# Performance work log

Hardware: AMD Instinct MI355X
Metric: run time of the kernel (lower is better)

Reference implementation:

```python
import jax, jax.numpy as jnp
import numpy as np

B, S, D, H = 4, 2048, 1024, 16
DH = D // H


def setup_inputs() -> dict:
    key = jax.random.key(0)
    ks = jax.random.split(key, 6)
    scale = 1.0 / np.sqrt(D)  # xavier-ish scale for weights
    return {
        "x": jax.random.normal(ks[0], (B, S, D), dtype=jnp.float32),
        "M": jax.random.normal(ks[1], (B, D, D), dtype=jnp.float32) * scale,
        "mask": jnp.zeros((1, 1, S, S), dtype=jnp.float32),
        "Wq": jax.random.normal(ks[2], (D, D), dtype=jnp.float32) * scale,
        "Wk": jax.random.normal(ks[3], (D, D), dtype=jnp.float32) * scale,
        "Wv": jax.random.normal(ks[4], (D, D), dtype=jnp.float32) * scale,
        "Wo": jax.random.normal(ks[5], (D, D), dtype=jnp.float32) * scale,
    }


def reference(x, M, mask, Wq, Wk, Wv, Wo):
    # Projections (torch Linear: y = x @ W^T, bias=False)
    Q = jnp.einsum('bsd,ed->bse', x, Wq)
    K = jnp.einsum('bsd,ed->bse', x, Wk)
    V = jnp.einsum('bsd,ed->bse', x, Wv)
    # Archetypal metric: QM = Q @ M, per-batch bilinear transform on full d_model
    QM = jnp.einsum('bsd,bde->bse', Q, M)

    def split(t):  # [B,S,D] -> [B,H,S,DH]
        return t.reshape(B, S, H, DH).transpose(0, 2, 1, 3)

    QMh, Kh, Vh = split(QM), split(K), split(V)
    scores = jnp.einsum('bhsd,bhtd->bhst', QMh, Kh) / np.sqrt(DH)
    scores = jnp.clip(scores, -50.0, 50.0)
    scores = scores + mask  # broadcast additive mask
    attn = jax.nn.softmax(scores, axis=-1)  # dropout is identity (eval)
    out = jnp.einsum('bhst,bhtd->bhsd', attn, Vh)
    out = out.transpose(0, 2, 1, 3).reshape(B, S, D)  # merge heads
    return jnp.einsum('bsd,ed->bse', out, Wo)
```

## Files before the change

kernel.cpp:

```cpp
#include <hip/hip_runtime.h>
#include <cstdint>

typedef __attribute__((ext_vector_type(8))) short short8;
typedef __attribute__((ext_vector_type(8))) __bf16 bf16x8;
typedef __attribute__((ext_vector_type(4))) float f32x4;

__device__ __forceinline__ uint32_t cvt_pk_bf16(float lo, float hi) {
  uint32_t r;
  asm("v_cvt_pk_bf16_f32 %0, %1, %2" : "=v"(r) : "v"(lo), "v"(hi));
  return r;
}

__device__ __forceinline__ short f2bf(float f) {
  return (short)cvt_pk_bf16(f, f);
}

__device__ __forceinline__ float exp2_fast(float x) {
  return __builtin_amdgcn_exp2f(x);
}

__device__ __forceinline__ void mem_fence_compiler() {
  asm volatile("" ::: "memory");
}

__device__ __forceinline__ void gload_lds16(const void* g, void* l) {
  __builtin_amdgcn_global_load_lds(
      (const __attribute__((address_space(1))) void*)(uintptr_t)g,
      (__attribute__((address_space(3))) void*)(uint32_t)(uintptr_t)l,
      16, 0, 0);
}


__global__ __launch_bounds__(256) void cvt_f32_bf16(const float* __restrict__ s,
                                                    short* __restrict__ d, long n) {
  long i = ((long)blockIdx.x * 256 + threadIdx.x) * 8;
  if (i + 8 > n) return;
  const float4 a = *(const float4*)(s + i);
  const float4 b = *(const float4*)(s + i + 4);
  uint4 o;
  o.x = cvt_pk_bf16(a.x, a.y);
  o.y = cvt_pk_bf16(a.z, a.w);
  o.z = cvt_pk_bf16(b.x, b.y);
  o.w = cvt_pk_bf16(b.z, b.w);
  *(uint4*)(d + i) = o;
}

__global__ __launch_bounds__(256) void cvt3_f32_bf16(
    const float* __restrict__ s0, short* __restrict__ d0,
    const float* __restrict__ s1, short* __restrict__ d1,
    const float* __restrict__ s2, short* __restrict__ d2) {
  const int which = blockIdx.x >> 9;
  const long i = (((long)(blockIdx.x & 511)) * 256 + threadIdx.x) * 8;
  const float* s = which == 0 ? s0 : (which == 1 ? s1 : s2);
  short* d = which == 0 ? d0 : (which == 1 ? d1 : d2);
  const float4 a = *(const float4*)(s + i);
  const float4 b = *(const float4*)(s + i + 4);
  uint4 o;
  o.x = cvt_pk_bf16(a.x, a.y);
  o.y = cvt_pk_bf16(a.z, a.w);
  o.z = cvt_pk_bf16(b.x, b.y);
  o.w = cvt_pk_bf16(b.z, b.w);
  *(uint4*)(d + i) = o;
}

__global__ __launch_bounds__(256) void cvtT5(const float* __restrict__ Wq,
                                             short* __restrict__ wqt,
                                             const float* __restrict__ M,
                                             short* __restrict__ Mt) {
  __shared__ short t[64][65];
  const int tid = threadIdx.x;
  const int z = blockIdx.z;
  const float* src = z == 0 ? Wq : M + (long)(z - 1) * 1024 * 1024;
  short* dst = z == 0 ? wqt : Mt + (long)(z - 1) * 1024 * 1024;
  const int d0 = blockIdx.x * 64, e0 = blockIdx.y * 64;
#pragma unroll
  for (int k = 0; k < 16; ++k) {
    int idx = k * 256 + tid; int r = idx >> 6, c = idx & 63;
    t[r][c] = f2bf(src[(long)(d0 + r) * 1024 + e0 + c]);
  }
  __syncthreads();
#pragma unroll
  for (int k = 0; k < 16; ++k) {
    int idx = k * 256 + tid; int r = idx >> 6, c = idx & 63;
    dst[(long)(e0 + r) * 1024 + d0 + c] = t[c][r];
  }
}

__global__ __launch_bounds__(256) void mask_flags(const float* __restrict__ mask,
                                                  int* __restrict__ flags) {
  __shared__ int f;
  const int tid = threadIdx.x;
  if (tid == 0) f = 0;
  __syncthreads();
  const int qt = blockIdx.x, tt = blockIdx.y;
  const float* base = mask + (long)qt * 64 * 2048 + tt * 64;
  const int r = tid >> 2, c = (tid & 3) * 16;
  bool nz = false;
#pragma unroll
  for (int k = 0; k < 4; ++k) {
    float4 v = *(const float4*)(base + (long)r * 2048 + c + k * 4);
    nz = nz | (v.x != 0.f) | (v.y != 0.f) | (v.z != 0.f) | (v.w != 0.f);
  }
  if (nz) f = 1;
  __syncthreads();
  if (tid == 0) flags[qt * 32 + tt] = f;
}


template <typename CT>
__global__ __launch_bounds__(256) void gemm_bt(
    const short* __restrict__ A, const short* __restrict__ B, CT* __restrict__ C,
    int M, int N, int K, long sA, long sB, long sC, float scale,
    short* __restrict__ vt) {
  __shared__ __align__(16) short pool[24576];
  short* Asb = pool;
  short* Bsb = pool + 12288;
  const int tid = threadIdx.x;
  const int w = tid >> 6, lane = tid & 63;
  const int wr = w >> 1, wc = w & 1;
  const int g = lane >> 4;
  const short* Ab = A + (long)blockIdx.z * sA + (long)blockIdx.x * 128 * K;
  const short* Bb = B + (long)blockIdx.z * sB + (long)blockIdx.y * 128 * K;

  f32x4 acc[4][4];
#pragma unroll
  for (int i = 0; i < 4; ++i)
#pragma unroll
    for (int j = 0; j < 4; ++j) acc[i][j] = {0.f, 0.f, 0.f, 0.f};

  const int srow = lane >> 2;
  const int scol = ((lane & 3) ^ (srow & 3)) * 8;

  auto STAGE = [&](int bufi, int k0) {
#pragma unroll
    for (int c = 0; c < 2; ++c) {
      const int chunk = w * 2 + c;
      const long gr = (long)(chunk * 16 + srow);
      gload_lds16(Ab + gr * K + k0 + scol, Asb + bufi * 4096 + chunk * 512);
      gload_lds16(Bb + gr * K + k0 + scol, Bsb + bufi * 4096 + chunk * 512);
    }
  };

  auto COMPUTE = [&](int bufi) {
    bf16x8 af[4], bfr[4];
#pragma unroll
    for (int mf = 0; mf < 4; ++mf) {
      const int r = wr * 64 + mf * 16 + (lane & 15);
      const int cb = g ^ (r & 3);
      af[mf] = *(const bf16x8*)&Asb[bufi * 4096 + r * 32 + cb * 8];
    }
#pragma unroll
    for (int nf = 0; nf < 4; ++nf) {
      const int r = wc * 64 + nf * 16 + (lane & 15);
      const int cb = g ^ (r & 3);
      bfr[nf] = *(const bf16x8*)&Bsb[bufi * 4096 + r * 32 + cb * 8];
    }
#pragma unroll
    for (int mf = 0; mf < 4; ++mf)
#pragma unroll
      for (int nf = 0; nf < 4; ++nf)
        acc[mf][nf] =
            __builtin_amdgcn_mfma_f32_16x16x32_bf16(af[mf], bfr[nf], acc[mf][nf], 0, 0, 0);
  };

  const int NK = K >> 5;
  STAGE(0, 0);
  if (NK > 1) STAGE(1, 32);
  for (int it = 0; it < NK; ++it) {
    const int cur = it % 3;
    if (it + 2 < NK) {
      STAGE((it + 2) % 3, (it + 2) * 32);
      asm volatile("s_waitcnt vmcnt(8)" ::: "memory");
    } else if (it + 1 < NK) {
      asm volatile("s_waitcnt vmcnt(4)" ::: "memory");
    } else {
      asm volatile("s_waitcnt vmcnt(0)" ::: "memory");
    }
    __builtin_amdgcn_s_barrier();
    __builtin_amdgcn_sched_barrier(0);
    COMPUTE(cur);
    __builtin_amdgcn_sched_barrier(0);
    __builtin_amdgcn_s_barrier();
  }

  const int r0 = g * 4, cc = lane & 15;
  if (vt != nullptr && blockIdx.z == 1) {
    __syncthreads();
#pragma unroll
    for (int mf = 0; mf < 4; ++mf)
#pragma unroll
      for (int i = 0; i < 4; ++i) {
        const int srow_l = wr * 64 + mf * 16 + r0 + i;
#pragma unroll
        for (int nf = 0; nf < 4; ++nf) {
          const int dh_l = wc * 64 + nf * 16 + cc;
          pool[dh_l * 136 + srow_l] = f2bf(acc[mf][nf][i]);
        }
      }
    __syncthreads();
    const long bb = blockIdx.x >> 4;
    const int s0b = (blockIdx.x & 15) * 128;
    const int hbase = blockIdx.y * 2;
#pragma unroll
    for (int pass = 0; pass < 4; ++pass) {
      const int dhrow = pass * 32 + (tid >> 3);
      const long vrow = (bb * 16 + hbase + (dhrow >> 6)) * 64 + (dhrow & 63);
      const int cseg = (tid & 7) * 16;
      bf16x8 v0 = *(const bf16x8*)&pool[dhrow * 136 + cseg];
      bf16x8 v1 = *(const bf16x8*)&pool[dhrow * 136 + cseg + 8];
      *(bf16x8*)(vt + vrow * 2048 + s0b + cseg) = v0;
      *(bf16x8*)(vt + vrow * 2048 + s0b + cseg + 8) = v1;
    }
    return;
  }

  CT* Cb = C + (long)blockIdx.z * sC;
#pragma unroll
  for (int mf = 0; mf < 4; ++mf)
#pragma unroll
    for (int i = 0; i < 4; ++i) {
      const long row = (long)blockIdx.x * 128 + wr * 64 + mf * 16 + r0 + i;
#pragma unroll
      for (int nf = 0; nf < 4; ++nf) {
        const long col = (long)blockIdx.y * 128 + wc * 64 + nf * 16 + cc;
        float v = acc[mf][nf][i] * scale;
        if constexpr (__is_same(CT, short))
          Cb[row * (long)N + col] = f2bf(v);
        else
          Cb[row * (long)N + col] = v;
      }
    }
}


__global__ __launch_bounds__(512) void flash_attn(
    const short* __restrict__ QM, const short* __restrict__ Kb,
    const short* __restrict__ Vt, const float* __restrict__ mask,
    const int* __restrict__ mflags, short* __restrict__ AO) {
  constexpr int S = 2048, D = 1024, NT = S / 64;
  constexpr float LOG2E = 1.44269504088896f;
  constexpr float CLIP = 50.0f * LOG2E;
  __shared__ __align__(16) short Ks[2][64 * 64];
  __shared__ __align__(16) short Vs[2][64 * 64];
  __shared__ __align__(16) short Ps[8][16 * 64];
  const int tid = threadIdx.x;
  const int w = tid >> 6, lane = tid & 63;
  const int q = lane & 15, g = lane >> 4;
  const int q0 = blockIdx.x * 128;
  const int h = blockIdx.y;
  const long b = blockIdx.z;

  const short* QMb = QM + (b * S) * D + h * 64;
  const short* Kbp = Kb + (b * S) * D + h * 64;
  const short* Vtp = Vt + ((b * 16 + h) * 64) * S;
  const int* flagrow = mflags + ((q0 + w * 16) >> 6) * 32;

  bf16x8 qf[2];
#pragma unroll
  for (int ks = 0; ks < 2; ++ks)
    qf[ks] = *(const bf16x8*)(QMb + (long)(q0 + w * 16 + q) * D + ks * 32 + g * 8);

  bf16x8 onesf;
#pragma unroll
  for (int j = 0; j < 8; ++j) onesf[j] = (__bf16)1.0f;

  f32x4 acc[4];
#pragma unroll
  for (int f = 0; f < 4; ++f) acc[f] = {0.f, 0.f, 0.f, 0.f};
  f32x4 acc_l = {0.f, 0.f, 0.f, 0.f};

  const int srow8 = lane >> 3;
  const int scol8 = ((lane & 7) ^ (srow8 & 7)) * 8;
  short* Pw = &Ps[w][0];
  const int psw = (q & 7) << 3;

  auto STAGE = [&](int bufi, int t0) {
    const int row = w * 8 + srow8;
    gload_lds16(Kbp + (long)(t0 + row) * D + scol8, &Ks[bufi][w * 512]);
    gload_lds16(Vtp + (long)row * S + t0 + scol8, &Vs[bufi][w * 512]);
  };

  auto COMPUTE = [&](int bufi, int t0) {
    f32x4 sacc[4];
#pragma unroll
    for (int nf = 0; nf < 4; ++nf) sacc[nf] = {0.f, 0.f, 0.f, 0.f};
    __builtin_amdgcn_s_setprio(1);
#pragma unroll
    for (int ks = 0; ks < 2; ++ks) {
#pragma unroll
      for (int nf = 0; nf < 4; ++nf) {
        const int r = nf * 16 + q;
        const int blk = (ks * 4 + g) ^ (r & 7);
        bf16x8 kf = *(const bf16x8*)&Ks[bufi][r * 64 + blk * 8];
        sacc[nf] = __builtin_amdgcn_mfma_f32_16x16x32_bf16(kf, qf[ks], sacc[nf], 0, 0, 0);
      }
    }
    __builtin_amdgcn_s_setprio(0);

    float pv[4][4];
    if (__builtin_expect(flagrow[t0 >> 6], 0)) {
      const float* mrow = mask + (long)(q0 + w * 16 + q) * S + t0;
#pragma unroll
      for (int nf = 0; nf < 4; ++nf) {
        float4 mv = *(const float4*)(mrow + nf * 16 + 4 * g);
        const float* mp = &mv.x;
#pragma unroll
        for (int i = 0; i < 4; ++i)
          pv[nf][i] = exp2_fast(
              __builtin_amdgcn_fmed3f(sacc[nf][i], -CLIP, CLIP) + LOG2E * mp[i]);
      }
    } else {
#pragma unroll
      for (int nf = 0; nf < 4; ++nf)
#pragma unroll
        for (int i = 0; i < 4; ++i)
          pv[nf][i] = exp2_fast(__builtin_amdgcn_fmed3f(sacc[nf][i], -CLIP, CLIP));
    }
#pragma unroll
    for (int nf = 0; nf < 4; ++nf) {
      uint2 u;
      u.x = cvt_pk_bf16(pv[nf][0], pv[nf][1]);
      u.y = cvt_pk_bf16(pv[nf][2], pv[nf][3]);
      *(uint2*)&Pw[q * 64 + ((nf * 16 + 4 * g) ^ psw)] = u;
    }

    mem_fence_compiler();

    __builtin_amdgcn_s_setprio(1);
#pragma unroll
    for (int ts = 0; ts < 2; ++ts) {
      bf16x8 pfr = *(const bf16x8*)&Pw[q * 64 + ((ts * 32 + 8 * g) ^ psw)];
#pragma unroll
      for (int f = 0; f < 4; ++f) {
        const int vr = f * 16 + q;
        const int vblk = (ts * 4 + g) ^ (vr & 7);
        bf16x8 vf = *(const bf16x8*)&Vs[bufi][vr * 64 + vblk * 8];
        acc[f] = __builtin_amdgcn_mfma_f32_16x16x32_bf16(vf, pfr, acc[f], 0, 0, 0);
      }
      acc_l = __builtin_amdgcn_mfma_f32_16x16x32_bf16(onesf, pfr, acc_l, 0, 0, 0);
    }
    __builtin_amdgcn_s_setprio(0);
    mem_fence_compiler();
  };

  STAGE(0, 0);
  for (int it = 0; it < NT; ++it) {
    const int cur = it & 1;
    if (it + 1 < NT) {
      STAGE(cur ^ 1, (it + 1) * 64);
      asm volatile("s_waitcnt vmcnt(2)" ::: "memory");
    } else {
      asm volatile("s_waitcnt vmcnt(0)" ::: "memory");
    }
    __builtin_amdgcn_s_barrier();
    __builtin_amdgcn_sched_barrier(0);
    COMPUTE(cur, it * 64);
    __builtin_amdgcn_sched_barrier(0);
    __builtin_amdgcn_s_barrier();
  }

  const float inv = 1.0f / acc_l[0];
#pragma unroll
  for (int f = 0; f < 4; ++f) {
    uint2 u;
    u.x = cvt_pk_bf16(acc[f][0] * inv, acc[f][1] * inv);
    u.y = cvt_pk_bf16(acc[f][2] * inv, acc[f][3] * inv);
    *(uint2*)&Pw[q * 64 + ((f * 16 + 4 * g) ^ psw)] = u;
  }
  mem_fence_compiler();
  const int qr = lane >> 2, c0 = (lane & 3) * 16;
  short* AOp = AO + (b * S) * D + h * 64;
#pragma unroll
  for (int r2 = 0; r2 < 2; ++r2) {
    const int cc2 = c0 + r2 * 8;
    bf16x8 ov = *(const bf16x8*)&Pw[qr * 64 + (cc2 ^ ((qr & 7) << 3))];
    *(bf16x8*)(AOp + (long)(q0 + w * 16 + qr) * D + cc2) = ov;
  }
}


extern "C" void kernel_launch(void* const* d_in, const int* in_sizes, int n_in,
                              void* d_out, int out_size, void* d_ws, size_t ws_size,
                              hipStream_t stream) {
  const float* x = (const float*)d_in[0];
  const float* M = (const float*)d_in[1];
  const float* mask = (const float*)d_in[2];
  const float* Wq = (const float*)d_in[3];
  const float* Wk = (const float*)d_in[4];
  const float* Wv = (const float*)d_in[5];
  const float* Wo = (const float*)d_in[6];
  float* out = (float*)d_out;

  constexpr long S = 2048, D = 1024;
  constexpr long NX = 4 * S * D;
  constexpr long NW = D * D;
  constexpr float C1 = 0.125f * 1.44269504088896f;

  short* p = (short*)d_ws;
  short* xb = p;   p += NX;
  short* wkb = p;  p += NW;
  short* wvb = p;  p += NW;
  short* wob = p;  p += NW;
  short* wqt = p;  p += NW;
  short* Mtb = p;  p += 4 * NW;
  short* Gtb = p;  p += 4 * NW;
  short* Kb = p;   p += NX;
  short* QMb = p;  p += NX;
  short* Vtb = p;  p += NX;
  int* flags = (int*)p;  p += 2048;
  short* AOb = Mtb;

  cvt_f32_bf16<<<NX / 2048, 256, 0, stream>>>(x, xb, NX);
  cvt3_f32_bf16<<<1536, 256, 0, stream>>>(Wk, wkb, Wv, wvb, Wo, wob);
  cvtT5<<<dim3(16, 16, 5), 256, 0, stream>>>(Wq, wqt, M, Mtb);
  mask_flags<<<dim3(32, 32), 256, 0, stream>>>(mask, flags);

  gemm_bt<short><<<dim3(64, 8, 2), 256, 0, stream>>>(xb, wkb, Kb, 8192, 1024, 1024,
                                                     0, NW, NX, 1.0f, Vtb);
  gemm_bt<short><<<dim3(8, 8, 4), 256, 0, stream>>>(Mtb, wqt, Gtb, 1024, 1024, 1024,
                                                    NW, 0, NW, 1.0f, nullptr);
  gemm_bt<short><<<dim3(16, 8, 4), 256, 0, stream>>>(xb, Gtb, QMb, 2048, 1024, 1024,
                                                     S * D, NW, S * D, C1, nullptr);
  flash_attn<<<dim3(16, 16, 4), 512, 0, stream>>>(QMb, Kb, Vtb, mask, flags, AOb);
  gemm_bt<float><<<dim3(64, 8, 1), 256, 0, stream>>>(AOb, wob, out, 8192, 1024, 1024,
                                                     0, 0, 0, 1.0f, nullptr);
}
```

Measured before the change: 236.1 us.

## Process two 16-row query tiles per wave to reuse staged K/V tiles

Each wave in flash_attn now handles 32 query rows as two independent 16-row sub-tiles, so each block covers 256 query rows and the grid is halved in x. Every K/V tile staged into LDS is reused for twice as many queries, which halves global K/V traffic and barrier count per query row. In exchange, per-thread register pressure roughly doubles and there are only 512 blocks, which may reduce occupancy and latency hiding.

```diff
diff --git a/kernel.cpp b/kernel.cpp
--- a/kernel.cpp
+++ b/kernel.cpp
@@ -246,28 +246,34 @@
   const int tid = threadIdx.x;
   const int w = tid >> 6, lane = tid & 63;
   const int q = lane & 15, g = lane >> 4;
-  const int q0 = blockIdx.x * 128;
+  const int q0 = blockIdx.x * 256;
   const int h = blockIdx.y;
   const long b = blockIdx.z;
 
   const short* QMb = QM + (b * S) * D + h * 64;
   const short* Kbp = Kb + (b * S) * D + h * 64;
   const short* Vtp = Vt + ((b * 16 + h) * 64) * S;
-  const int* flagrow = mflags + ((q0 + w * 16) >> 6) * 32;
-
-  bf16x8 qf[2];
-#pragma unroll
-  for (int ks = 0; ks < 2; ++ks)
-    qf[ks] = *(const bf16x8*)(QMb + (long)(q0 + w * 16 + q) * D + ks * 32 + g * 8);
+  const int qw = q0 + w * 32;
+
+  bf16x8 qf0[2], qf1[2];
+#pragma unroll
+  for (int ks = 0; ks < 2; ++ks) {
+    qf0[ks] = *(const bf16x8*)(QMb + (long)(qw + q) * D + ks * 32 + g * 8);
+    qf1[ks] = *(const bf16x8*)(QMb + (long)(qw + 16 + q) * D + ks * 32 + g * 8);
+  }
 
   bf16x8 onesf;
 #pragma unroll
   for (int j = 0; j < 8; ++j) onesf[j] = (__bf16)1.0f;
 
-  f32x4 acc[4];
-#pragma unroll
-  for (int f = 0; f < 4; ++f) acc[f] = {0.f, 0.f, 0.f, 0.f};
-  f32x4 acc_l = {0.f, 0.f, 0.f, 0.f};
+  f32x4 accA[4], accB[4];
+#pragma unroll
+  for (int f = 0; f < 4; ++f) {
+    accA[f] = {0.f, 0.f, 0.f, 0.f};
+    accB[f] = {0.f, 0.f, 0.f, 0.f};
+  }
+  f32x4 acc_lA = {0.f, 0.f, 0.f, 0.f};
+  f32x4 acc_lB = {0.f, 0.f, 0.f, 0.f};
 
   const int srow8 = lane >> 3;
   const int scol8 = ((lane & 7) ^ (srow8 & 7)) * 8;
@@ -280,7 +286,8 @@
     gload_lds16(Vtp + (long)row * S + t0 + scol8, &Vs[bufi][w * 512]);
   };
 
-  auto COMPUTE = [&](int bufi, int t0) {
+  auto COMPUTE_U = [&](int bufi, int t0, int qrow, const bf16x8 (&qf)[2],
+                       f32x4 (&acc)[4], f32x4& acc_l) {
     f32x4 sacc[4];
 #pragma unroll
     for (int nf = 0; nf < 4; ++nf) sacc[nf] = {0.f, 0.f, 0.f, 0.f};
@@ -298,8 +305,9 @@
     __builtin_amdgcn_s_setprio(0);
 
     float pv[4][4];
-    if (__builtin_expect(flagrow[t0 >> 6], 0)) {
-      const float* mrow = mask + (long)(q0 + w * 16 + q) * S + t0;
+    const int* flagrowU = mflags + (qrow >> 6) * 32;
+    if (__builtin_expect(flagrowU[t0 >> 6], 0)) {
+      const float* mrow = mask + (long)(qrow + q) * S + t0;
 #pragma unroll
       for (int nf = 0; nf < 4; ++nf) {
         float4 mv = *(const float4*)(mrow + nf * 16 + 4 * g);
@@ -354,27 +362,33 @@
     }
     __builtin_amdgcn_s_barrier();
     __builtin_amdgcn_sched_barrier(0);
-    COMPUTE(cur, it * 64);
+    COMPUTE_U(cur, it * 64, qw, qf0, accA, acc_lA);
+    COMPUTE_U(cur, it * 64, qw + 16, qf1, accB, acc_lB);
     __builtin_amdgcn_sched_barrier(0);
     __builtin_amdgcn_s_barrier();
   }
 
-  const float inv = 1.0f / acc_l[0];
-#pragma unroll
-  for (int f = 0; f < 4; ++f) {
-    uint2 u;
-    u.x = cvt_pk_bf16(acc[f][0] * inv, acc[f][1] * inv);
-    u.y = cvt_pk_bf16(acc[f][2] * inv, acc[f][3] * inv);
-    *(uint2*)&Pw[q * 64 + ((f * 16 + 4 * g) ^ psw)] = u;
-  }
-  mem_fence_compiler();
   const int qr = lane >> 2, c0 = (lane & 3) * 16;
   short* AOp = AO + (b * S) * D + h * 64;
 #pragma unroll
-  for (int r2 = 0; r2 < 2; ++r2) {
-    const int cc2 = c0 + r2 * 8;
-    bf16x8 ov = *(const bf16x8*)&Pw[qr * 64 + (cc2 ^ ((qr & 7) << 3))];
-    *(bf16x8*)(AOp + (long)(q0 + w * 16 + qr) * D + cc2) = ov;
+  for (int u = 0; u < 2; ++u) {
+    const f32x4* acc = (u == 0) ? accA : accB;
+    const float inv = 1.0f / ((u == 0) ? acc_lA[0] : acc_lB[0]);
+#pragma unroll
+    for (int f = 0; f < 4; ++f) {
+      uint2 uu;
+      uu.x = cvt_pk_bf16(acc[f][0] * inv, acc[f][1] * inv);
+      uu.y = cvt_pk_bf16(acc[f][2] * inv, acc[f][3] * inv);
+      *(uint2*)&Pw[q * 64 + ((f * 16 + 4 * g) ^ psw)] = uu;
+    }
+    mem_fence_compiler();
+#pragma unroll
+    for (int r2 = 0; r2 < 2; ++r2) {
+      const int cc2 = c0 + r2 * 8;
+      bf16x8 ov = *(const bf16x8*)&Pw[qr * 64 + (cc2 ^ ((qr & 7) << 3))];
+      *(bf16x8*)(AOp + (long)(qw + u * 16 + qr) * D + cc2) = ov;
+    }
+    mem_fence_compiler();
   }
 }
 
@@ -421,7 +435,7 @@
                                                     NW, 0, NW, 1.0f, nullptr);
   gemm_bt<short><<<dim3(16, 8, 4), 256, 0, stream>>>(xb, Gtb, QMb, 2048, 1024, 1024,
                                                      S * D, NW, S * D, C1, nullptr);
-  flash_attn<<<dim3(16, 16, 4), 512, 0, stream>>>(QMb, Kb, Vtb, mask, flags, AOb);
+  flash_attn<<<dim3(8, 16, 4), 512, 0, stream>>>(QMb, Kb, Vtb, mask, flags, AOb);
   gemm_bt<float><<<dim3(64, 8, 1), 256, 0, stream>>>(AOb, wob, out, 8192, 1024, 1024,
                                                      0, 0, 0, 1.0f, nullptr);
 }
```

New measurement: 228.0 us. 3.4% less time.
